# Optimization experiments

Hardware: AMD Instinct MI355X
Metric: run time of the kernel (lower is better)

## Reference

```python
import jax, jax.numpy as jnp
import numpy as np

D_MODEL = 2048
NUM_HEADS = 32
NUM_KV_HEADS = 8
D_K = D_MODEL // NUM_HEADS  # 64
GROUPS = NUM_HEADS // NUM_KV_HEADS  # 4
ROPE_BASE = 10000.0


def rope_cos_sin(n, dim):
    # RotaryPositionalEmbedding.forward: freqs = t outer inv_freq; emb = cat(freqs, freqs)
    inv_freq = 1.0 / (ROPE_BASE ** (jnp.arange(0, dim, 2, dtype=jnp.float32) / dim))
    t = jnp.arange(n, dtype=jnp.float32)
    freqs = jnp.einsum('i,j->ij', t, inv_freq)  # [n, dim/2]
    emb = jnp.concatenate([freqs, freqs], axis=-1)  # [n, dim]
    return jnp.cos(emb), jnp.sin(emb)


def rotate_half(x):
    x1, x2 = x[..., : x.shape[-1] // 2], x[..., x.shape[-1] // 2:]
    return jnp.concatenate([-x2, x1], axis=-1)


def setup_inputs() -> dict:
    key = jax.random.key(0)
    k0, k1, k2, k3, k4 = jax.random.split(key, 5)
    B, N = 1, 2048
    x = jax.random.normal(k0, (B, N, D_MODEL), dtype=jnp.float32)
    s = 0.02
    Wq = jax.random.normal(k1, (D_MODEL, D_MODEL), dtype=jnp.float32) * s
    Wk = jax.random.normal(k2, (D_MODEL, NUM_KV_HEADS * D_K), dtype=jnp.float32) * s
    Wv = jax.random.normal(k3, (D_MODEL, NUM_KV_HEADS * D_K), dtype=jnp.float32) * s
    Wo = jax.random.normal(k4, (D_MODEL, D_MODEL), dtype=jnp.float32) * s
    return {'x': x, 'Wq': Wq, 'Wk': Wk, 'Wv': Wv, 'Wo': Wo}


def reference(x, Wq, Wk, Wv, Wo):
    B, N, C = x.shape
    scale = D_K ** -0.5
    # projections -> [B, H, N, d_k]
    q = (x @ Wq).reshape(B, N, NUM_HEADS, D_K).transpose(0, 2, 1, 3)
    k = (x @ Wk).reshape(B, N, NUM_KV_HEADS, D_K).transpose(0, 2, 1, 3)
    v = (x @ Wv).reshape(B, N, NUM_KV_HEADS, D_K).transpose(0, 2, 1, 3)
    # GQA: repeat_interleave KV heads to match Q heads
    k = jnp.repeat(k, GROUPS, axis=1)
    v = jnp.repeat(v, GROUPS, axis=1)
    cos, sin = rope_cos_sin(N, D_K)  # [N, d_k]
    cos = cos[None, None, :, :]
    sin = sin[None, None, :, :]
    q = q * cos + rotate_half(q) * sin
    k = k * cos + rotate_half(k) * sin
    attn = jnp.einsum('bhnd,bhmd->bhnm', q, k) * scale  # [B, H, N, N]
    attn = jax.nn.softmax(attn, axis=-1)
    out = jnp.einsum('bhnm,bhmd->bhnd', attn, v)  # [B, H, N, d_k]
    out = out.transpose(0, 2, 1, 3).reshape(B, N, C)
    out = out @ Wo
    return out, attn
```

## Files before the change

kernel.cpp:

```cpp
#include <hip/hip_runtime.h>

typedef _Float16 f16x8 __attribute__((ext_vector_type(8)));
typedef _Float16 f16x4 __attribute__((ext_vector_type(4)));
typedef _Float16 f16x2 __attribute__((ext_vector_type(2)));
typedef float f32x4 __attribute__((ext_vector_type(4)));

#define NSEQ 2048
#define DMODEL 2048
#define NHEADS 32
#define NKV 8
#define DK 64
#define MFMA16(a, b, c) __builtin_amdgcn_mfma_f32_16x16x32_f16(a, b, c, 0, 0, 0)

__device__ __forceinline__ void gload16(const void* g, void* l) {
    __builtin_amdgcn_global_load_lds(
        (const __attribute__((address_space(1))) void*)g,
        (__attribute__((address_space(3))) void*)l, 16, 0, 0);
}

__global__ void cvt_f32_f16(const float* __restrict__ in, _Float16* __restrict__ out, int n4) {
    int i = blockIdx.x * blockDim.x + threadIdx.x;
    int stride = gridDim.x * blockDim.x;
    for (; i < n4; i += stride) {
        float4 v = ((const float4*)in)[i];
        f16x4 h;
        h[0] = (_Float16)v.x; h[1] = (_Float16)v.y;
        h[2] = (_Float16)v.z; h[3] = (_Float16)v.w;
        ((f16x4*)out)[i] = h;
    }
}

__global__ __launch_bounds__(256) void transpose_cvt(const float* __restrict__ in,
                                                     _Float16* __restrict__ out,
                                                     int R, int C) {
    __shared__ float tile[32][33];
    int c0 = blockIdx.x * 32, r0 = blockIdx.y * 32;
    int tx = threadIdx.x, ty = threadIdx.y;
#pragma unroll
    for (int i = 0; i < 4; i++) {
        int r = r0 + ty + i * 8;
        tile[ty + i * 8][tx] = in[(long long)r * C + c0 + tx];
    }
    __syncthreads();
#pragma unroll
    for (int i = 0; i < 4; i++) {
        int c = c0 + ty + i * 8;
        out[(long long)c * R + r0 + tx] = (_Float16)tile[tx][ty + i * 8];
    }
}

__global__ __launch_bounds__(256) void transpose16p(const _Float16* __restrict__ in,
                                                    _Float16* __restrict__ out,
                                                    int R, int C, int pitch) {
    __shared__ _Float16 tile[32][34];
    int c0 = blockIdx.x * 32, r0 = blockIdx.y * 32;
    int tx = threadIdx.x, ty = threadIdx.y;
#pragma unroll
    for (int i = 0; i < 4; i++) {
        int r = r0 + ty + i * 8;
        tile[ty + i * 8][tx] = in[(long long)r * pitch + c0 + tx];
    }
    __syncthreads();
#pragma unroll
    for (int i = 0; i < 4; i++) {
        int c = c0 + ty + i * 8;
        out[(long long)c * R + r0 + tx] = tile[tx][ty + i * 8];
    }
}

__global__ void rope_table(float2* __restrict__ cs) {
    int idx = blockIdx.x * blockDim.x + threadIdx.x;
    int n = idx >> 5, j = idx & 31;
    float e = (2.0f * j) / 64.0f;
    float invf = 1.0f / powf(10000.0f, e);
    float ang = (float)n * invf;
    float2 v; v.x = cosf(ang); v.y = sinf(ang);
    cs[idx] = v;
}

__global__ void rope_apply16(const _Float16* __restrict__ QKV, const float2* __restrict__ cs,
                             _Float16* __restrict__ out) {
    int idx = blockIdx.x * blockDim.x + threadIdx.x;
    int n = idx >> 8, rem = idx & 255;
    int hk = rem >> 5, j = rem & 31;
    float2 c = cs[n * 32 + j];
    const _Float16* in = QKV + (long long)n * 3072 + 2048 + hk * 64;
    float x1 = (float)in[j], x2 = (float)in[j + 32];
    long long ob = (long long)n * 512 + hk * 64;
    out[ob + j]      = (_Float16)(x1 * c.x - x2 * c.y);
    out[ob + j + 32] = (_Float16)(x2 * c.x + x1 * c.y);
}

template <int BM, int BN, int MF, int NF, typename OutT>
__global__ __launch_bounds__(256) void gemm_lds(const _Float16* __restrict__ Ap,
                                                const _Float16* __restrict__ Bt,
                                                OutT* __restrict__ C,
                                                int K, int lda, int ldb, int ldc) {
    __shared__ __align__(16) _Float16 As[BM * 32];
    __shared__ __align__(16) _Float16 Bs[BN * 32];

    const int tid = threadIdx.x;
    const int lane = tid & 63, w = tid >> 6;
    constexpr int WC = BN / (NF * 16);
    const int wr = w / WC, wc = w % WC;
    const int wm = wr * MF * 16, wn = wc * NF * 16;
    const int am = lane & 15;
    const int g = lane >> 4;

    f32x4 acc[MF][NF] = {};

    const long long a_row0 = (long long)blockIdx.y * BM * lda;
    const long long b_row0 = (long long)blockIdx.x * BN * ldb;

    const int srow = lane >> 2;
    const int scol = (lane & 3) * 8;

    for (int kt = 0; kt < K; kt += 32) {
#pragma unroll
        for (int q = 0; q < BM / 64; q++) {
            const int row = w * (BM / 4) + q * 16 + srow;
            gload16(Ap + a_row0 + (long long)row * lda + kt + scol,
                    &As[w * (BM * 8) + q * 512]);
        }
#pragma unroll
        for (int q = 0; q < BN / 64; q++) {
            const int row = w * (BN / 4) + q * 16 + srow;
            gload16(Bt + b_row0 + (long long)row * ldb + kt + scol,
                    &Bs[w * (BN * 8) + q * 512]);
        }
        __syncthreads();

        f16x8 af[MF], bf[NF];
#pragma unroll
        for (int m = 0; m < MF; m++) af[m] = *(const f16x8*)&As[(wm + m * 16 + am) * 32 + g * 8];
#pragma unroll
        for (int n = 0; n < NF; n++) bf[n] = *(const f16x8*)&Bs[(wn + n * 16 + am) * 32 + g * 8];
#pragma unroll
        for (int m = 0; m < MF; m++)
#pragma unroll
            for (int n = 0; n < NF; n++)
                acc[m][n] = MFMA16(af[m], bf[n], acc[m][n]);
        __syncthreads();
    }

    const int rb = blockIdx.y * BM + wm + (lane >> 4) * 4;
    const int cb = blockIdx.x * BN + wn + am;
#pragma unroll
    for (int m = 0; m < MF; m++)
#pragma unroll
        for (int n = 0; n < NF; n++)
#pragma unroll
            for (int j = 0; j < 4; j++)
                C[(long long)(rb + m * 16 + j) * ldc + cb + n * 16] = (OutT)acc[m][n][j];
}

__global__ __launch_bounds__(512) void attn_sums(
    const _Float16* __restrict__ QKV,
    const float2*  __restrict__ cs,
    const _Float16* __restrict__ Kh,
    float* __restrict__ Sinv)
{
    __shared__ __align__(16) char LB[32768];

    const int h = blockIdx.y, q0 = blockIdx.x * 128;
    const int kvh = h >> 2;
    const int tid = threadIdx.x, lane = tid & 63, w = tid >> 6;
    const int g = lane >> 4, c = lane & 15;
    const int swz = (c & 7) << 4;

    const _Float16* qp = QKV + (long long)(q0 + w * 16 + c) * 3072 + h * 64;
    f16x8 q0v = *(const f16x8*)(qp + g * 8);
    f16x8 q1v = *(const f16x8*)(qp + 32 + g * 8);
    const float2* csp = cs + (q0 + w * 16 + c) * 32 + g * 8;
    f16x8 qa, qb_;
#pragma unroll
    for (int e = 0; e < 8; e++) {
        float2 cv = csp[e];
        float x1 = (float)q0v[e], x2 = (float)q1v[e];
        qa[e]  = (_Float16)(x1 * cv.x - x2 * cv.y);
        qb_[e] = (_Float16)(x2 * cv.x + x1 * cv.y);
    }

    const _Float16* Kg = Kh + kvh * 64;
    const int krl = lane >> 3, kcb = (lane & 7) * 16;

#pragma unroll
    for (int q = 0; q < 2; q++) {
        int r = w * 16 + q * 8 + krl;
        gload16(Kg + (long long)r * 512 + ((kcb ^ ((r & 7) << 4)) >> 1),
                LB + (w * 16 + q * 8) * 128);
    }
    __syncthreads();

    float l = 0.f;
    for (int i = 0; i < 16; i++) {
        const char* kbuf = LB + (i & 1) * 16384;
        char* kstage = LB + ((i & 1) ^ 1) * 16384;
        const int nkc = ((i + 1) & 15) * 128;
#pragma unroll
        for (int q = 0; q < 2; q++) {
            int r = w * 16 + q * 8 + krl;
            gload16(Kg + (long long)(nkc + r) * 512 + ((kcb ^ ((r & 7) << 4)) >> 1),
                    kstage + (w * 16 + q * 8) * 128);
        }
#pragma unroll
        for (int t = 0; t < 8; t++) {
            const char* kb = kbuf + (t * 16 + c) * 128;
            f16x8 kb0 = *(const f16x8*)(kb + ((g * 16) ^ swz));
            f16x8 kb1 = *(const f16x8*)(kb + ((64 + g * 16) ^ swz));
            f32x4 acc = {0.f, 0.f, 0.f, 0.f};
            acc = MFMA16(kb0, qa, acc);
            acc = MFMA16(kb1, qb_, acc);
            l += __expf(fminf(acc[0] * 0.125f, 11.f)) + __expf(fminf(acc[1] * 0.125f, 11.f)) +
                 __expf(fminf(acc[2] * 0.125f, 11.f)) + __expf(fminf(acc[3] * 0.125f, 11.f));
        }
        __syncthreads();
    }
    l += __shfl_xor(l, 16, 64);
    l += __shfl_xor(l, 32, 64);
    if (lane < 16)
        Sinv[(long long)h * NSEQ + q0 + w * 16 + c] = 1.0f / l;
}

__global__ __launch_bounds__(512) void fused_attn(
    const _Float16* __restrict__ QKV,
    const float2*  __restrict__ cs,
    const _Float16* __restrict__ Kh,
    const _Float16* __restrict__ Vt,
    const float* __restrict__ Sinv,
    float* __restrict__ attn,
    _Float16* __restrict__ AVh)
{
    __shared__ __align__(16) char LB[81920];

    const int h = blockIdx.y, q0 = blockIdx.x * 128;
    const int kvh = h >> 2;
    const int tid = threadIdx.x, lane = tid & 63, w = tid >> 6;
    const int g = lane >> 4, c = lane & 15;
    const int swz = (c & 7) << 4;

    const _Float16* qp = QKV + (long long)(q0 + w * 16 + c) * 3072 + h * 64;
    f16x8 q0v = *(const f16x8*)(qp + g * 8);
    f16x8 q1v = *(const f16x8*)(qp + 32 + g * 8);
    const float2* csp = cs + (q0 + w * 16 + c) * 32 + g * 8;
    f16x8 qa, qb_;
#pragma unroll
    for (int e = 0; e < 8; e++) {
        float2 cv = csp[e];
        float x1 = (float)q0v[e], x2 = (float)q1v[e];
        qa[e]  = (_Float16)(x1 * cv.x - x2 * cv.y);
        qb_[e] = (_Float16)(x2 * cv.x + x1 * cv.y);
    }

    const float inv = Sinv[(long long)h * NSEQ + q0 + w * 16 + c];

    const _Float16* Kg = Kh + kvh * 64;
    const _Float16* Vg = Vt + (long long)(kvh * 64) * NSEQ;
    char* ES = LB + 49152 + w * 4096;
    float* arow0 = attn + ((long long)h * NSEQ + q0 + w * 16) * NSEQ;

    const int krl = lane >> 3, kcb = (lane & 7) * 16;
    const int vrl = lane >> 4, vcb = (lane & 15) * 16;

#pragma unroll
    for (int q = 0; q < 2; q++) {
        int r = w * 16 + q * 8 + krl;
        gload16(Kg + (long long)r * 512 + ((kcb ^ ((r & 7) << 4)) >> 1),
                LB + (w * 16 + q * 8) * 128);
    }
    __syncthreads();

    f32x4 opv[4] = {};

    for (int i = 0; i < 16; i++) {
        const int kc = i * 128;
        const char* kbuf = LB + (i & 1) * 16384;
        char* kstage = LB + ((i & 1) ^ 1) * 16384;
        const int nkc = ((i + 1) & 15) * 128;
#pragma unroll
        for (int q = 0; q < 2; q++) {
            int r = w * 16 + q * 8 + krl;
            gload16(Kg + (long long)(nkc + r) * 512 + ((kcb ^ ((r & 7) << 4)) >> 1),
                    kstage + (w * 16 + q * 8) * 128);
        }
#pragma unroll
        for (int q = 0; q < 2; q++) {
            int j = w + q * 8;
            int d = j * 4 + vrl;
            gload16(Vg + (long long)d * NSEQ + kc + ((vcb ^ ((d & 7) << 4)) >> 1),
                    LB + 32768 + j * 1024);
        }
#pragma unroll
        for (int t = 0; t < 4; t++) {
            const char* kb = kbuf + (t * 16 + c) * 128;
            f16x8 kb0 = *(const f16x8*)(kb + ((g * 16) ^ swz));
            f16x8 kb1 = *(const f16x8*)(kb + ((64 + g * 16) ^ swz));
            f32x4 acc = {0.f, 0.f, 0.f, 0.f};
            acc = MFMA16(kb0, qa, acc);
            acc = MFMA16(kb1, qb_, acc);
            float p0 = __expf(fminf(acc[0] * 0.125f, 11.f)) * inv;
            float p1 = __expf(fminf(acc[1] * 0.125f, 11.f)) * inv;
            float p2 = __expf(fminf(acc[2] * 0.125f, 11.f)) * inv;
            float p3 = __expf(fminf(acc[3] * 0.125f, 11.f)) * inv;
            f16x2 a01; a01[0] = (_Float16)p0; a01[1] = (_Float16)p1;
            f16x2 a23; a23[0] = (_Float16)p2; a23[1] = (_Float16)p3;
            int b0 = c * 256 + ((t * 32 + g * 8) ^ swz);
            *(f16x2*)(ES + b0) = a01;
            *(f16x2*)(ES + b0 + 4) = a23;
        }
        __asm__ volatile("s_waitcnt lgkmcnt(0)" ::: "memory");
        f16x8 pa0 = *(const f16x8*)(ES + c * 256 + ((g * 16) ^ swz));
        f16x8 pa1 = *(const f16x8*)(ES + c * 256 + ((64 + g * 16) ^ swz));
        __syncthreads();
#pragma unroll
        for (int dt = 0; dt < 4; dt++) {
            const char* vrow = LB + 32768 + (dt * 16 + c) * 256;
            f16x8 vb0 = *(const f16x8*)(vrow + ((g * 16) ^ swz));
            f16x8 vb1 = *(const f16x8*)(vrow + ((64 + g * 16) ^ swz));
            opv[dt] = MFMA16(pa0, vb0, opv[dt]);
            opv[dt] = MFMA16(pa1, vb1, opv[dt]);
        }
#pragma unroll
        for (int t = 4; t < 8; t++) {
            const char* kb = kbuf + (t * 16 + c) * 128;
            f16x8 kb0 = *(const f16x8*)(kb + ((g * 16) ^ swz));
            f16x8 kb1 = *(const f16x8*)(kb + ((64 + g * 16) ^ swz));
            f32x4 acc = {0.f, 0.f, 0.f, 0.f};
            acc = MFMA16(kb0, qa, acc);
            acc = MFMA16(kb1, qb_, acc);
            float p0 = __expf(fminf(acc[0] * 0.125f, 11.f)) * inv;
            float p1 = __expf(fminf(acc[1] * 0.125f, 11.f)) * inv;
            float p2 = __expf(fminf(acc[2] * 0.125f, 11.f)) * inv;
            float p3 = __expf(fminf(acc[3] * 0.125f, 11.f)) * inv;
            f16x2 a01; a01[0] = (_Float16)p0; a01[1] = (_Float16)p1;
            f16x2 a23; a23[0] = (_Float16)p2; a23[1] = (_Float16)p3;
            int b0 = c * 256 + ((t * 32 + g * 8) ^ swz);
            *(f16x2*)(ES + b0) = a01;
            *(f16x2*)(ES + b0 + 4) = a23;
        }
        __asm__ volatile("s_waitcnt lgkmcnt(0)" ::: "memory");
        f16x8 pa2 = *(const f16x8*)(ES + c * 256 + ((128 + g * 16) ^ swz));
        f16x8 pa3 = *(const f16x8*)(ES + c * 256 + ((192 + g * 16) ^ swz));
#pragma unroll
        for (int rr = 0; rr < 8; rr++) {
            const int r = 2 * rr + (lane >> 5);
            f16x4 ev = *(const f16x4*)(ES + r * 256 + (((lane & 31) * 8) ^ ((r & 7) << 4)));
            f32x4 o;
            o[0] = (float)ev[0]; o[1] = (float)ev[1];
            o[2] = (float)ev[2]; o[3] = (float)ev[3];
            *(f32x4*)(arow0 + (long long)r * NSEQ + kc + (lane & 31) * 4) = o;
        }
#pragma unroll
        for (int dt = 0; dt < 4; dt++) {
            const char* vrow = LB + 32768 + (dt * 16 + c) * 256;
            f16x8 vb2 = *(const f16x8*)(vrow + ((128 + g * 16) ^ swz));
            f16x8 vb3 = *(const f16x8*)(vrow + ((192 + g * 16) ^ swz));
            opv[dt] = MFMA16(pa2, vb2, opv[dt]);
            opv[dt] = MFMA16(pa3, vb3, opv[dt]);
        }
        __syncthreads();
    }

#pragma unroll
    for (int dt = 0; dt < 4; dt++)
#pragma unroll
        for (int j = 0; j < 4; j++)
            AVh[(long long)(q0 + w * 16 + 4 * g + j) * DMODEL + h * 64 + dt * 16 + c] =
                (_Float16)opv[dt][j];
}

extern "C" void kernel_launch(void* const* d_in, const int* in_sizes, int n_in,
                              void* d_out, int out_size, void* d_ws, size_t ws_size,
                              hipStream_t stream) {
    const float* x  = (const float*)d_in[0];
    const float* Wq = (const float*)d_in[1];
    const float* Wk = (const float*)d_in[2];
    const float* Wv = (const float*)d_in[3];
    const float* Wo = (const float*)d_in[4];
    float* out = (float*)d_out;
    float* attn = out + (size_t)NSEQ * DMODEL;

    char* w = (char*)d_ws;
    auto alloc = [&](size_t bytes) { char* p = w; w += (bytes + 255) & ~(size_t)255; return p; };
    const size_t MD = (size_t)NSEQ * DMODEL;
    const size_t MKV = (size_t)NSEQ * NKV * DK;
    _Float16* xh    = (_Float16*)alloc(MD * 2);
    _Float16* WqkvT = (_Float16*)alloc((size_t)3072 * 2048 * 2);
    _Float16* WoT   = (_Float16*)alloc(MD * 2);
    float2*   cs    = (float2*)alloc((size_t)NSEQ * 32 * sizeof(float2));
    _Float16* QKV   = (_Float16*)alloc((size_t)2048 * 3072 * 2);
    _Float16* Kh    = (_Float16*)alloc(MKV * 2);
    _Float16* Vt    = (_Float16*)alloc(MKV * 2);
    float*    Sinv  = (float*)alloc((size_t)NHEADS * NSEQ * 4);
    _Float16* AVh   = xh;

    cvt_f32_f16<<<2048, 256, 0, stream>>>(x, xh, (int)(MD / 4));
    transpose_cvt<<<dim3(64, 64), dim3(32, 8), 0, stream>>>(Wq, WqkvT, DMODEL, DMODEL);
    transpose_cvt<<<dim3(16, 64), dim3(32, 8), 0, stream>>>(Wk, WqkvT + (size_t)2048 * 2048, DMODEL, 512);
    transpose_cvt<<<dim3(16, 64), dim3(32, 8), 0, stream>>>(Wv, WqkvT + (size_t)2560 * 2048, DMODEL, 512);
    transpose_cvt<<<dim3(64, 64), dim3(32, 8), 0, stream>>>(Wo, WoT, DMODEL, DMODEL);
    rope_table<<<256, 256, 0, stream>>>(cs);

    gemm_lds<128, 128, 4, 4, _Float16><<<dim3(24, 16), 256, 0, stream>>>(
        xh, WqkvT, QKV, DMODEL, DMODEL, DMODEL, 3072);

    rope_apply16<<<2048, 256, 0, stream>>>(QKV, cs, Kh);
    transpose16p<<<dim3(16, 64), dim3(32, 8), 0, stream>>>(QKV + 2560, Vt, NSEQ, 512, 3072);

    attn_sums<<<dim3(NSEQ / 128, NHEADS), 512, 0, stream>>>(QKV, cs, Kh, Sinv);

    fused_attn<<<dim3(NSEQ / 128, NHEADS), 512, 0, stream>>>(QKV, cs, Kh, Vt, Sinv, attn, AVh);

    gemm_lds<128, 128, 4, 4, float><<<dim3(16, 16), 256, 0, stream>>>(
        AVh, WoT, out, DMODEL, DMODEL, DMODEL, DMODEL);
}
```

Baseline: 302.7 us.

## Merge prep kernels and rework GEMM with 64-wide K tiles and XOR swizzle

```diff
diff --git a/kernel.cpp b/kernel.cpp
--- a/kernel.cpp
+++ b/kernel.cpp
@@ -18,24 +18,30 @@
         (__attribute__((address_space(3))) void*)l, 16, 0, 0);
 }
 
-__global__ void cvt_f32_f16(const float* __restrict__ in, _Float16* __restrict__ out, int n4) {
-    int i = blockIdx.x * blockDim.x + threadIdx.x;
-    int stride = gridDim.x * blockDim.x;
-    for (; i < n4; i += stride) {
-        float4 v = ((const float4*)in)[i];
-        f16x4 h;
-        h[0] = (_Float16)v.x; h[1] = (_Float16)v.y;
-        h[2] = (_Float16)v.z; h[3] = (_Float16)v.w;
-        ((f16x4*)out)[i] = h;
-    }
-}
-
-__global__ __launch_bounds__(256) void transpose_cvt(const float* __restrict__ in,
-                                                     _Float16* __restrict__ out,
-                                                     int R, int C) {
+__global__ __launch_bounds__(256) void prep_weights(
+    const float* __restrict__ x,  const float* __restrict__ Wq,
+    const float* __restrict__ Wk, const float* __restrict__ Wv,
+    const float* __restrict__ Wo, _Float16* __restrict__ xh,
+    _Float16* __restrict__ WqkvT, _Float16* __restrict__ WoT) {
+    const int z = blockIdx.z;
+    const int tx = threadIdx.x, ty = threadIdx.y;
+    if (z == 0) {
+        int c0 = blockIdx.x * 32, r0 = blockIdx.y * 32;
+#pragma unroll
+        for (int i = 0; i < 4; i++) {
+            int r = r0 + ty + i * 8;
+            xh[(long long)r * DMODEL + c0 + tx] = (_Float16)x[(long long)r * DMODEL + c0 + tx];
+        }
+        return;
+    }
+    const float* in; _Float16* out; int C;
+    if (z == 1)      { in = Wq; out = WqkvT;                        C = 2048; }
+    else if (z == 2) { in = Wk; out = WqkvT + (size_t)2048 * 2048;  C = 512;  }
+    else if (z == 3) { in = Wv; out = WqkvT + (size_t)2560 * 2048;  C = 512;  }
+    else             { in = Wo; out = WoT;                          C = 2048; }
+    int c0 = blockIdx.x * 32, r0 = blockIdx.y * 32;
+    if (c0 >= C) return;
     __shared__ float tile[32][33];
-    int c0 = blockIdx.x * 32, r0 = blockIdx.y * 32;
-    int tx = threadIdx.x, ty = threadIdx.y;
 #pragma unroll
     for (int i = 0; i < 4; i++) {
         int r = r0 + ty + i * 8;
@@ -45,7 +51,7 @@
 #pragma unroll
     for (int i = 0; i < 4; i++) {
         int c = c0 + ty + i * 8;
-        out[(long long)c * R + r0 + tx] = (_Float16)tile[tx][ty + i * 8];
+        out[(long long)c * 2048 + r0 + tx] = (_Float16)tile[tx][ty + i * 8];
     }
 }
 
@@ -92,12 +98,12 @@
 }
 
 template <int BM, int BN, int MF, int NF, typename OutT>
-__global__ __launch_bounds__(256) void gemm_lds(const _Float16* __restrict__ Ap,
-                                                const _Float16* __restrict__ Bt,
-                                                OutT* __restrict__ C,
-                                                int K, int lda, int ldb, int ldc) {
-    __shared__ __align__(16) _Float16 As[BM * 32];
-    __shared__ __align__(16) _Float16 Bs[BN * 32];
+__global__ __launch_bounds__(256) void gemm_lds2(const _Float16* __restrict__ Ap,
+                                                 const _Float16* __restrict__ Bt,
+                                                 OutT* __restrict__ C,
+                                                 int K, int lda, int ldb, int ldc) {
+    __shared__ __align__(16) _Float16 As[BM * 64];
+    __shared__ __align__(16) _Float16 Bs[BN * 64];
 
     const int tid = threadIdx.x;
     const int lane = tid & 63, w = tid >> 6;
@@ -106,40 +112,49 @@
     const int wm = wr * MF * 16, wn = wc * NF * 16;
     const int am = lane & 15;
     const int g = lane >> 4;
+    const int aswz = (am & 7) << 4;
 
     f32x4 acc[MF][NF] = {};
 
     const long long a_row0 = (long long)blockIdx.y * BM * lda;
     const long long b_row0 = (long long)blockIdx.x * BN * ldb;
 
-    const int srow = lane >> 2;
-    const int scol = (lane & 3) * 8;
-
-    for (int kt = 0; kt < K; kt += 32) {
-#pragma unroll
-        for (int q = 0; q < BM / 64; q++) {
-            const int row = w * (BM / 4) + q * 16 + srow;
-            gload16(Ap + a_row0 + (long long)row * lda + kt + scol,
-                    &As[w * (BM * 8) + q * 512]);
-        }
-#pragma unroll
-        for (int q = 0; q < BN / 64; q++) {
-            const int row = w * (BN / 4) + q * 16 + srow;
-            gload16(Bt + b_row0 + (long long)row * ldb + kt + scol,
-                    &Bs[w * (BN * 8) + q * 512]);
+    const int srow = lane >> 3;
+    const int scolb = (lane & 7) * 16;
+
+    for (int kt = 0; kt < K; kt += 64) {
+#pragma unroll
+        for (int q = 0; q < BM / 32; q++) {
+            const int rA = w * (BM / 4) + q * 8;
+            const int r = rA + srow;
+            gload16(Ap + a_row0 + (long long)r * lda + kt + ((scolb ^ ((r & 7) << 4)) >> 1),
+                    &As[rA * 64]);
+        }
+#pragma unroll
+        for (int q = 0; q < BN / 32; q++) {
+            const int rB = w * (BN / 4) + q * 8;
+            const int r = rB + srow;
+            gload16(Bt + b_row0 + (long long)r * ldb + kt + ((scolb ^ ((r & 7) << 4)) >> 1),
+                    &Bs[rB * 64]);
         }
         __syncthreads();
 
-        f16x8 af[MF], bf[NF];
-#pragma unroll
-        for (int m = 0; m < MF; m++) af[m] = *(const f16x8*)&As[(wm + m * 16 + am) * 32 + g * 8];
-#pragma unroll
-        for (int n = 0; n < NF; n++) bf[n] = *(const f16x8*)&Bs[(wn + n * 16 + am) * 32 + g * 8];
-#pragma unroll
-        for (int m = 0; m < MF; m++)
+#pragma unroll
+        for (int ks = 0; ks < 2; ks++) {
+            const int koff = ((ks * 64 + g * 16) ^ aswz) >> 1;
+            f16x8 af[MF], bf[NF];
+#pragma unroll
+            for (int m = 0; m < MF; m++)
+                af[m] = *(const f16x8*)&As[(wm + m * 16 + am) * 64 + koff];
 #pragma unroll
             for (int n = 0; n < NF; n++)
-                acc[m][n] = MFMA16(af[m], bf[n], acc[m][n]);
+                bf[n] = *(const f16x8*)&Bs[(wn + n * 16 + am) * 64 + koff];
+#pragma unroll
+            for (int m = 0; m < MF; m++)
+#pragma unroll
+                for (int n = 0; n < NF; n++)
+                    acc[m][n] = MFMA16(af[m], bf[n], acc[m][n]);
+        }
         __syncthreads();
     }
 
@@ -394,14 +409,11 @@
     float*    Sinv  = (float*)alloc((size_t)NHEADS * NSEQ * 4);
     _Float16* AVh   = xh;
 
-    cvt_f32_f16<<<2048, 256, 0, stream>>>(x, xh, (int)(MD / 4));
-    transpose_cvt<<<dim3(64, 64), dim3(32, 8), 0, stream>>>(Wq, WqkvT, DMODEL, DMODEL);
-    transpose_cvt<<<dim3(16, 64), dim3(32, 8), 0, stream>>>(Wk, WqkvT + (size_t)2048 * 2048, DMODEL, 512);
-    transpose_cvt<<<dim3(16, 64), dim3(32, 8), 0, stream>>>(Wv, WqkvT + (size_t)2560 * 2048, DMODEL, 512);
-    transpose_cvt<<<dim3(64, 64), dim3(32, 8), 0, stream>>>(Wo, WoT, DMODEL, DMODEL);
+    prep_weights<<<dim3(64, 64, 5), dim3(32, 8), 0, stream>>>(
+        x, Wq, Wk, Wv, Wo, xh, WqkvT, WoT);
     rope_table<<<256, 256, 0, stream>>>(cs);
 
-    gemm_lds<128, 128, 4, 4, _Float16><<<dim3(24, 16), 256, 0, stream>>>(
+    gemm_lds2<128, 64, 4, 2, _Float16><<<dim3(48, 16), 256, 0, stream>>>(
         xh, WqkvT, QKV, DMODEL, DMODEL, DMODEL, 3072);
 
     rope_apply16<<<2048, 256, 0, stream>>>(QKV, cs, Kh);
@@ -411,6 +423,6 @@
 
     fused_attn<<<dim3(NSEQ / 128, NHEADS), 512, 0, stream>>>(QKV, cs, Kh, Vt, Sinv, attn, AVh);
 
-    gemm_lds<128, 128, 4, 4, float><<<dim3(16, 16), 256, 0, stream>>>(
+    gemm_lds2<128, 64, 4, 2, float><<<dim3(32, 16), 256, 0, stream>>>(
         AVh, WoT, out, DMODEL, DMODEL, DMODEL, DMODEL);
 }
```

Result: faster. 264.0 us (-12.8%).
